# Kernel optimization log

Measured on AMD Instinct MI355X. Metric: run time of the kernel, lower is better.

The kernel has to match this reference:

```python
import jax, jax.numpy as jnp
import numpy as np

N_NODES = 100000
N_EDGES = 1000000
N_FEAT = 136
HIDDEN = 64
N_CLASSES = 2
NUM_GRAPHS = 512


def setup_inputs() -> dict:
    key = jax.random.key(0)
    ks = jax.random.split(key, 8)
    x = jax.random.normal(ks[0], (N_NODES, N_FEAT), dtype=jnp.float32)
    edge_index = jax.random.randint(ks[1], (2, N_EDGES), 0, N_NODES, dtype=jnp.int64)
    batch = jnp.sort(jax.random.randint(ks[2], (N_NODES,), 0, NUM_GRAPHS, dtype=jnp.int64))
    W1 = jax.random.normal(ks[3], (N_FEAT, HIDDEN), dtype=jnp.float32) * (1.0 / np.sqrt(N_FEAT))
    b1 = jnp.zeros((HIDDEN,), dtype=jnp.float32)
    W2 = jax.random.normal(ks[4], (HIDDEN, HIDDEN), dtype=jnp.float32) * (1.0 / np.sqrt(HIDDEN))
    b2 = jnp.zeros((HIDDEN,), dtype=jnp.float32)
    Wout = jax.random.normal(ks[5], (HIDDEN, N_CLASSES), dtype=jnp.float32) * (1.0 / np.sqrt(HIDDEN))
    bout = jnp.zeros((N_CLASSES,), dtype=jnp.float32)
    return {"x": x, "edge_index": edge_index, "batch": batch,
            "W1": W1, "b1": b1, "W2": W2, "b2": b2, "Wout": Wout, "bout": bout}


def _gcn_conv(x, src, dst, W, b, n_nodes):
    # GCNConv: D^{-1/2} (A+I) D^{-1/2} X W + b (self-loops already appended in src/dst)
    h = x @ W                                           # [N, out]
    ones = jnp.ones(src.shape, dtype=h.dtype)
    deg = jax.ops.segment_sum(ones, dst, num_segments=n_nodes)  # in-degree incl. self-loop
    dinv = jnp.where(deg > 0, jax.lax.rsqrt(deg), 0.0)
    norm = dinv[src] * dinv[dst]                        # [E]
    msg = h[src] * norm[:, None]                        # gather + normalize
    out = jax.ops.segment_sum(msg, dst, num_segments=n_nodes)   # scatter-add
    return out + b


def reference(x, edge_index, batch, W1, b1, W2, b2, Wout, bout):
    n = x.shape[0]
    loops = jnp.arange(n, dtype=edge_index.dtype)
    src = jnp.concatenate([edge_index[0], loops])
    dst = jnp.concatenate([edge_index[1], loops])

    h = jax.nn.relu(_gcn_conv(x, src, dst, W1, b1, n))
    # dropout p=0.5 is identity in eval mode
    h = jax.nn.relu(_gcn_conv(h, src, dst, W2, b2, n))

    # global_mean_pool over batch segments
    sums = jax.ops.segment_sum(h, batch, num_segments=NUM_GRAPHS)       # [G, H]
    counts = jax.ops.segment_sum(jnp.ones((n,), h.dtype), batch, num_segments=NUM_GRAPHS)
    pooled = sums / jnp.maximum(counts, 1.0)[:, None]

    return pooled @ Wout + bout                                         # [G, C]
```

## Files before the change

kernel.cpp:

```cpp
#include <hip/hip_runtime.h>
#include <hip/hip_bf16.h>

#define N_NODES   100000
#define N_EDGES   1000000
#define N_FEAT    136
#define HIDDEN    64
#define N_CLASSES 2
#define NUM_GRAPHS 512

#define NP_PAD    100352
#define SCAN_BLKS 98

#define EPW       128
#define NWAVE     7813
#define E_PAD     (NWAVE * EPW)
#define SEG_BLOCKS ((NWAVE + 3) / 4)

#define XCD        8
#define PART_N     (N_NODES / XCD)

#define K1_4 (N_FEAT / 4)
#define K2_4 (HIDDEN / 4)

#define K1PAD 160
#define K2PAD 72

typedef unsigned short ushort_t;
typedef __attribute__((ext_vector_type(8))) short bf16x8;
typedef __attribute__((ext_vector_type(4))) float f32x4;

__device__ __forceinline__ ushort_t f2b(float v) {
    unsigned b = __float_as_uint(v);
    return (ushort_t)((b + 0x7FFF + ((b >> 16) & 1)) >> 16);
}
__device__ __forceinline__ float b2f(ushort_t u) {
    return __uint_as_float(((unsigned)u) << 16);
}
__device__ __forceinline__ unsigned pack2(float a, float b) {
    return (unsigned)f2b(a) | ((unsigned)f2b(b) << 16);
}

__global__ __launch_bounds__(256) void hist_kernel(const int* __restrict__ dst,
                                                   int* __restrict__ cnt) {
    int e = blockIdx.x * 256 + threadIdx.x;
    if (e < N_EDGES) {
        int d = __builtin_nontemporal_load(&dst[e]);
        atomicAdd(&cnt[d], 1);
    }
}

__global__ __launch_bounds__(256) void scan1_kernel(const int* __restrict__ cnt,
                                                    int* __restrict__ row_ptr,
                                                    int* __restrict__ partials) {
    __shared__ int sd[256];
    int b = blockIdx.x, t = threadIdx.x;
    int i0 = b * 1024 + t * 4;
    int c0 = (i0 + 0 < N_NODES) ? cnt[i0 + 0] : 0;
    int c1 = (i0 + 1 < N_NODES) ? cnt[i0 + 1] : 0;
    int c2 = (i0 + 2 < N_NODES) ? cnt[i0 + 2] : 0;
    int c3 = (i0 + 3 < N_NODES) ? cnt[i0 + 3] : 0;
    int tsum = c0 + c1 + c2 + c3;
    sd[t] = tsum;
    __syncthreads();
    for (int off = 1; off < 256; off <<= 1) {
        int v = (t >= off) ? sd[t - off] : 0;
        __syncthreads();
        sd[t] += v;
        __syncthreads();
    }
    int excl = sd[t] - tsum;
    row_ptr[i0 + 0] = excl;
    row_ptr[i0 + 1] = excl + c0;
    row_ptr[i0 + 2] = excl + c0 + c1;
    row_ptr[i0 + 3] = excl + c0 + c1 + c2;
    if (t == 255) partials[b] = sd[255];
}

__global__ __launch_bounds__(128) void scan2_kernel(int* __restrict__ partials) {
    __shared__ int sd[128];
    int t = threadIdx.x;
    int v = (t < SCAN_BLKS) ? partials[t] : 0;
    sd[t] = v;
    __syncthreads();
    for (int off = 1; off < 128; off <<= 1) {
        int u = (t >= off) ? sd[t - off] : 0;
        __syncthreads();
        sd[t] += u;
        __syncthreads();
    }
    partials[t] = sd[t] - v;
}

__global__ __launch_bounds__(256) void scan3_kernel(int* __restrict__ row_ptr,
                                                    const int* __restrict__ cnt,
                                                    int* __restrict__ cursor,
                                                    const int* __restrict__ partials,
                                                    int* __restrict__ dst_sorted,
                                                    int* __restrict__ csr_src,
                                                    float* __restrict__ dinv) {
    int i = blockIdx.x * 256 + threadIdx.x;
    if (i < N_NODES) {
        int v = row_ptr[i] + partials[i >> 10];
        int deg = cnt[i];
        row_ptr[i] = v;
        cursor[i]  = v;
        dinv[i] = rsqrtf((float)(deg + 1));
        for (int j = v; j < v + deg; ++j) dst_sorted[j] = i;
    }
    if (i == N_NODES) {
        row_ptr[N_NODES] = N_EDGES;
        for (int j = N_EDGES; j < E_PAD; ++j) {
            dst_sorted[j] = N_NODES;
            csr_src[j] = 0;
        }
    }
}

__global__ __launch_bounds__(256) void scatter_kernel(const int* __restrict__ src,
                                                      const int* __restrict__ dst,
                                                      int* __restrict__ cursor,
                                                      int* __restrict__ csr_src) {
    int part = blockIdx.x & (XCD - 1);
    int e = (blockIdx.x >> 3) * 256 + threadIdx.x;
    if (e >= N_EDGES) return;
    int d = __builtin_nontemporal_load(&dst[e]);
    int lo = part * PART_N;
    if (d >= lo && d < lo + PART_N) {
        int s = __builtin_nontemporal_load(&src[e]);
        int pos = atomicAdd(&cursor[d], 1);
        csr_src[pos] = s;
    }
}

__global__ __launch_bounds__(256) void gbounds_kernel(const int* __restrict__ batch,
                                                      int* __restrict__ gstart) {
    int g = blockIdx.x * 256 + threadIdx.x;
    if (g > NUM_GRAPHS) return;
    int lo = 0, hi = N_NODES;
    while (lo < hi) {
        int mid = (lo + hi) >> 1;
        if (batch[mid] < g) lo = mid + 1; else hi = mid;
    }
    gstart[g] = lo;
}

__global__ __launch_bounds__(256) void mm1_kernel(const float* __restrict__ x,
                                                  const float* __restrict__ W1,
                                                  const float* __restrict__ dinv,
                                                  ushort_t* __restrict__ tpb) {
    __shared__ ushort_t xsb[64 * K1PAD];
    __shared__ ushort_t wtb[64 * K1PAD];
    __shared__ float    dsv[64];
    int t = threadIdx.x;
    int n0 = blockIdx.x * 64;
    {
        const float4* x4 = (const float4*)x;
        for (int i = t; i < 64 * K1_4; i += 256) {
            int r = i / K1_4, c = i % K1_4;
            int n = n0 + r; if (n >= N_NODES) n = N_NODES - 1;
            float4 v = x4[(long long)n * K1_4 + c];
            *(uint2*)&xsb[r * K1PAD + 4 * c] =
                make_uint2(pack2(v.x, v.y), pack2(v.z, v.w));
        }
        for (int i = t; i < 64 * 12; i += 256) {
            int r = i / 12, c = i % 12;
            *(unsigned*)&xsb[r * K1PAD + N_FEAT + 2 * c] = 0;
        }
        for (int i = t; i < N_FEAT * HIDDEN; i += 256) {
            int n = i & 63, k = i >> 6;
            wtb[n * K1PAD + k] = f2b(W1[i]);
        }
        for (int i = t; i < 64 * 12; i += 256) {
            int n = i / 12, c = i % 12;
            *(unsigned*)&wtb[n * K1PAD + N_FEAT + 2 * c] = 0;
        }
        if (t < 64) {
            int n = n0 + t; if (n >= N_NODES) n = N_NODES - 1;
            dsv[t] = dinv[n];
        }
    }
    __syncthreads();
    int w = t >> 6, lane = t & 63;
    int quad = lane >> 4, l16 = lane & 15;
    f32x4 acc[4] = {{0,0,0,0},{0,0,0,0},{0,0,0,0},{0,0,0,0}};
#pragma unroll
    for (int kc = 0; kc < K1PAD / 32; ++kc) {
        bf16x8 a = *(const bf16x8*)&xsb[(w * 16 + l16) * K1PAD + kc * 32 + quad * 8];
#pragma unroll
        for (int nt = 0; nt < 4; ++nt) {
            bf16x8 b = *(const bf16x8*)&wtb[(nt * 16 + l16) * K1PAD + kc * 32 + quad * 8];
            acc[nt] = __builtin_amdgcn_mfma_f32_16x16x32_bf16(a, b, acc[nt], 0, 0, 0);
        }
    }
#pragma unroll
    for (int r = 0; r < 4; ++r) {
        int nl = w * 16 + quad * 4 + r;
        int node = n0 + nl;
        if (node < N_NODES) {
            float di = dsv[nl];
#pragma unroll
            for (int nt = 0; nt < 4; ++nt)
                tpb[node * 64 + nt * 16 + l16] = f2b(acc[nt][r] * di);
        }
    }
}

__global__ __launch_bounds__(256) void mm2_kernel(float* __restrict__ agg,
                                                  ushort_t* __restrict__ tpb,
                                                  const float* __restrict__ W2,
                                                  const float* __restrict__ dinv,
                                                  const float* __restrict__ bias) {
    __shared__ ushort_t hsb[64 * K2PAD];
    __shared__ ushort_t wtb[64 * K2PAD];
    __shared__ float    dsv[64];
    __shared__ float    bsv[64];
    int t = threadIdx.x;
    int n0 = blockIdx.x * 64;
    if (t < 64) {
        int n = n0 + t; if (n >= N_NODES) n = N_NODES - 1;
        dsv[t] = dinv[n];
        bsv[t] = bias[t];
    }
    __syncthreads();
    {
        for (int i = t; i < HIDDEN * HIDDEN; i += 256) {
            int n = i & 63, k = i >> 6;
            wtb[n * K2PAD + k] = f2b(W2[i]);
        }
        for (int i = t; i < 64 * 4; i += 256) {
            int n = i / 4, c = i % 4;
            *(unsigned*)&wtb[n * K2PAD + HIDDEN + 2 * c] = 0;
        }
        for (int i = t; i < 64 * 16; i += 256) {
            int r = i >> 4, c = i & 15;
            int n_raw = n0 + r;
            int n = (n_raw < N_NODES) ? n_raw : N_NODES - 1;
            float4 va = ((const float4*)agg)[n * 16 + c];
            uint2 ut = *(const uint2*)&tpb[n * 64 + c * 4];
            float di = dsv[r];
            float s0 = b2f((ushort_t)(ut.x & 0xffff));
            float s1 = b2f((ushort_t)(ut.x >> 16));
            float s2 = b2f((ushort_t)(ut.y & 0xffff));
            float s3 = b2f((ushort_t)(ut.y >> 16));
            float h0 = fmaxf(fmaf(va.x + s0, di, bsv[c * 4 + 0]), 0.f);
            float h1 = fmaxf(fmaf(va.y + s1, di, bsv[c * 4 + 1]), 0.f);
            float h2 = fmaxf(fmaf(va.z + s2, di, bsv[c * 4 + 2]), 0.f);
            float h3 = fmaxf(fmaf(va.w + s3, di, bsv[c * 4 + 3]), 0.f);
            *(uint2*)&hsb[r * K2PAD + 4 * c] = make_uint2(pack2(h0, h1), pack2(h2, h3));
            if (n_raw < N_NODES)
                ((float4*)agg)[n * 16 + c] = make_float4(0.f, 0.f, 0.f, 0.f);
        }
        for (int i = t; i < 64 * 4; i += 256) {
            int r = i / 4, c = i % 4;
            *(unsigned*)&hsb[r * K2PAD + HIDDEN + 2 * c] = 0;
        }
    }
    __syncthreads();
    int w = t >> 6, lane = t & 63;
    int quad = lane >> 4, l16 = lane & 15;
    f32x4 acc[4] = {{0,0,0,0},{0,0,0,0},{0,0,0,0},{0,0,0,0}};
#pragma unroll
    for (int kc = 0; kc < 2; ++kc) {
        bf16x8 a = *(const bf16x8*)&hsb[(w * 16 + l16) * K2PAD + kc * 32 + quad * 8];
#pragma unroll
        for (int nt = 0; nt < 4; ++nt) {
            bf16x8 b = *(const bf16x8*)&wtb[(nt * 16 + l16) * K2PAD + kc * 32 + quad * 8];
            acc[nt] = __builtin_amdgcn_mfma_f32_16x16x32_bf16(a, b, acc[nt], 0, 0, 0);
        }
    }
#pragma unroll
    for (int r = 0; r < 4; ++r) {
        int nl = w * 16 + quad * 4 + r;
        int node = n0 + nl;
        if (node < N_NODES) {
            float di = dsv[nl];
#pragma unroll
            for (int nt = 0; nt < 4; ++nt)
                tpb[node * 64 + nt * 16 + l16] = f2b(acc[nt][r] * di);
        }
    }
}

__global__ __launch_bounds__(256, 4) void edge_seg_kernel(const int* __restrict__ csr_src,
                                                          const int* __restrict__ dst_sorted,
                                                          const ushort_t* __restrict__ tpb,
                                                          float* __restrict__ agg) {
    int lane = threadIdx.x & 63;
    int wid  = (blockIdx.x * 256 + threadIdx.x) >> 6;
    if (wid >= NWAVE) return;
    int e0 = wid * EPW;

    int sv0 = csr_src[e0 + lane],      sv1 = csr_src[e0 + 64 + lane];
    int dv0 = dst_sorted[e0 + lane],   dv1 = dst_sorted[e0 + 64 + lane];

    float acc = 0.0f;
    int dprev = __builtin_amdgcn_readlane(dv0, 0);
    int nflush = 0;
#pragma unroll
    for (int j = 0; j < 8; ++j) {
        int svj = (j < 4) ? sv0 : sv1;
        int dvj = (j < 4) ? dv0 : dv1;
        int base = (j * 16) & 63;
        int ss[16], dd[16];
#pragma unroll
        for (int k = 0; k < 16; ++k) {
            ss[k] = __builtin_amdgcn_readlane(svj, base + k);
            dd[k] = __builtin_amdgcn_readlane(dvj, base + k);
        }
        float vv[16];
#pragma unroll
        for (int k = 0; k < 16; ++k) vv[k] = b2f(tpb[ss[k] * 64 + lane]);
#pragma unroll
        for (int k = 0; k < 16; ++k) {
            if (dd[k] != dprev) {
                if (nflush == 0) atomicAdd(&agg[dprev * 64 + lane], acc);
                else             agg[dprev * 64 + lane] = acc;
                ++nflush;
                acc = 0.0f;
                dprev = dd[k];
            }
            acc += vv[k];
        }
    }
    atomicAdd(&agg[dprev * 64 + lane], acc);
}

__global__ __launch_bounds__(256) void gpool_kernel(const float* __restrict__ agg,
                                                    const ushort_t* __restrict__ tpb,
                                                    const float* __restrict__ dinv,
                                                    const float* __restrict__ bias,
                                                    const int* __restrict__ gstart,
                                                    float* __restrict__ sums,
                                                    float* __restrict__ gcount) {
    __shared__ float red[4][64];
    int lane = threadIdx.x & 63;
    int w = threadIdx.x >> 6;
    int g = blockIdx.x;
    int s = gstart[g], e = gstart[g + 1];
    float b = bias[lane];
    float acc = 0.0f;
    for (int n = s + w; n < e; n += 4) {
        int idx = n * 64 + lane;
        acc += fmaxf(fmaf(agg[idx] + b2f(tpb[idx]), dinv[n], b), 0.0f);
    }
    red[w][lane] = acc;
    __syncthreads();
    if (threadIdx.x < 64) {
        float tot = red[0][lane] + red[1][lane] + red[2][lane] + red[3][lane];
        sums[g * 64 + lane] = tot;
        if (lane == 0) gcount[g] = (float)(e - s);
    }
}

__global__ __launch_bounds__(256) void out_kernel(const float* __restrict__ sums,
                                                  const float* __restrict__ gcount,
                                                  const float* __restrict__ Wout,
                                                  const float* __restrict__ bout,
                                                  float* __restrict__ out) {
    int idx = blockIdx.x * 256 + threadIdx.x;
    if (idx >= NUM_GRAPHS * N_CLASSES) return;
    int g = idx / N_CLASSES, c = idx % N_CLASSES;
    float inv_cnt = 1.0f / fmaxf(gcount[g], 1.0f);
    float acc = 0.0f;
#pragma unroll
    for (int k = 0; k < HIDDEN; ++k)
        acc += sums[g * HIDDEN + k] * Wout[k * N_CLASSES + c];
    out[idx] = acc * inv_cnt + bout[c];
}

extern "C" void kernel_launch(void* const* d_in, const int* in_sizes, int n_in,
                              void* d_out, int out_size, void* d_ws, size_t ws_size,
                              hipStream_t stream) {
    const float* x     = (const float*)d_in[0];
    const int*   ei    = (const int*)d_in[1];
    const int*   batch = (const int*)d_in[2];
    const float* W1    = (const float*)d_in[3];
    const float* b1    = (const float*)d_in[4];
    const float* W2    = (const float*)d_in[5];
    const float* b2    = (const float*)d_in[6];
    const float* Wout  = (const float*)d_in[7];
    const float* bout  = (const float*)d_in[8];
    float* out = (float*)d_out;

    const int* src = ei;
    const int* dst = ei + N_EDGES;

    char* p = (char*)d_ws;
    int*      row_ptr   = (int*)p;      p += (NP_PAD + 256) * sizeof(int);
    int*      cnt       = (int*)p;      p += NP_PAD * sizeof(int);
    int*      cursor    = (int*)p;      p += NP_PAD * sizeof(int);
    int*      partials  = (int*)p;      p += 256 * sizeof(int);
    int*      gstart    = (int*)p;      p += (NUM_GRAPHS + 64) * sizeof(int);
    int*      csr_src   = (int*)p;      p += (size_t)E_PAD * sizeof(int);
    int*      dst_sorted= (int*)p;      p += (size_t)E_PAD * sizeof(int);
    float*    dinv      = (float*)p;    p += NP_PAD * sizeof(float);
    ushort_t* tpb       = (ushort_t*)p; p += (size_t)N_NODES * HIDDEN * sizeof(ushort_t);
    float*    agg       = (float*)p;    p += (size_t)(N_NODES + 1) * HIDDEN * sizeof(float);
    float*    sums      = (float*)p;    p += NUM_GRAPHS * HIDDEN * sizeof(float);
    float*    gcount    = (float*)p;    p += NUM_GRAPHS * sizeof(float);

    const int NB_E  = (N_EDGES + 255) / 256;
    const int NB_MM = (N_NODES + 63) / 64;

    hipMemsetAsync(cnt, 0, NP_PAD * sizeof(int), stream);
    hist_kernel<<<NB_E, 256, 0, stream>>>(dst, cnt);
    scan1_kernel<<<SCAN_BLKS, 256, 0, stream>>>(cnt, row_ptr, partials);
    scan2_kernel<<<1, 128, 0, stream>>>(partials);
    scan3_kernel<<<NP_PAD / 256 + 1, 256, 0, stream>>>(row_ptr, cnt, cursor, partials,
                                                       dst_sorted, csr_src, dinv);
    scatter_kernel<<<XCD * NB_E, 256, 0, stream>>>(src, dst, cursor, csr_src);
    gbounds_kernel<<<3, 256, 0, stream>>>(batch, gstart);

    hipMemsetAsync(agg, 0, (size_t)(N_NODES + 1) * HIDDEN * sizeof(float), stream);

    mm1_kernel<<<NB_MM, 256, 0, stream>>>(x, W1, dinv, tpb);
    edge_seg_kernel<<<SEG_BLOCKS, 256, 0, stream>>>(csr_src, dst_sorted, tpb, agg);

    mm2_kernel<<<NB_MM, 256, 0, stream>>>(agg, tpb, W2, dinv, b1);
    edge_seg_kernel<<<SEG_BLOCKS, 256, 0, stream>>>(csr_src, dst_sorted, tpb, agg);
    gpool_kernel<<<NUM_GRAPHS, 256, 0, stream>>>(agg, tpb, dinv, b2, gstart,
                                                 sums, gcount);

    out_kernel<<<(NUM_GRAPHS * N_CLASSES + 255) / 256, 256, 0, stream>>>(
        sums, gcount, Wout, bout, out);
}
```

Baseline: 310.0 us.

## Record edge ranks in histogram to make CSR scatter atomic-free, fuse small kernels

```diff
diff --git a/kernel.cpp b/kernel.cpp
--- a/kernel.cpp
+++ b/kernel.cpp
@@ -16,18 +16,20 @@
 #define E_PAD     (NWAVE * EPW)
 #define SEG_BLOCKS ((NWAVE + 3) / 4)
 
-#define XCD        8
-#define PART_N     (N_NODES / XCD)
-
 #define K1_4 (N_FEAT / 4)
 #define K2_4 (HIDDEN / 4)
 
 #define K1PAD 160
 #define K2PAD 72
+
+#define NB_E  ((N_EDGES + 255) / 256)
+#define NB_SC ((N_EDGES / 4 + 255) / 256)
 
 typedef unsigned short ushort_t;
 typedef __attribute__((ext_vector_type(8))) short bf16x8;
 typedef __attribute__((ext_vector_type(4))) float f32x4;
+typedef __attribute__((ext_vector_type(4))) int i32x4;
+typedef __attribute__((ext_vector_type(4))) unsigned short u16x4;
 
 __device__ __forceinline__ ushort_t f2b(float v) {
     unsigned b = __float_as_uint(v);
@@ -41,11 +43,27 @@
 }
 
 __global__ __launch_bounds__(256) void hist_kernel(const int* __restrict__ dst,
-                                                   int* __restrict__ cnt) {
+                                                   int* __restrict__ cnt,
+                                                   ushort_t* __restrict__ rank,
+                                                   const int* __restrict__ batch,
+                                                   int* __restrict__ gstart) {
+    if (blockIdx.x >= NB_E) {
+        int g = (blockIdx.x - NB_E) * 256 + threadIdx.x;
+        if (g <= NUM_GRAPHS) {
+            int lo = 0, hi = N_NODES;
+            while (lo < hi) {
+                int mid = (lo + hi) >> 1;
+                if (batch[mid] < g) lo = mid + 1; else hi = mid;
+            }
+            gstart[g] = lo;
+        }
+        return;
+    }
     int e = blockIdx.x * 256 + threadIdx.x;
     if (e < N_EDGES) {
         int d = __builtin_nontemporal_load(&dst[e]);
-        atomicAdd(&cnt[d], 1);
+        int r = atomicAdd(&cnt[d], 1);
+        rank[e] = (ushort_t)r;
     }
 }
 
@@ -93,7 +111,6 @@
 
 __global__ __launch_bounds__(256) void scan3_kernel(int* __restrict__ row_ptr,
                                                     const int* __restrict__ cnt,
-                                                    int* __restrict__ cursor,
                                                     const int* __restrict__ partials,
                                                     int* __restrict__ dst_sorted,
                                                     int* __restrict__ csr_src,
@@ -103,7 +120,6 @@
         int v = row_ptr[i] + partials[i >> 10];
         int deg = cnt[i];
         row_ptr[i] = v;
-        cursor[i]  = v;
         dinv[i] = rsqrtf((float)(deg + 1));
         for (int j = v; j < v + deg; ++j) dst_sorted[j] = i;
     }
@@ -118,42 +134,41 @@
 
 __global__ __launch_bounds__(256) void scatter_kernel(const int* __restrict__ src,
                                                       const int* __restrict__ dst,
-                                                      int* __restrict__ cursor,
+                                                      const ushort_t* __restrict__ rank,
+                                                      const int* __restrict__ row_ptr,
                                                       int* __restrict__ csr_src) {
-    int part = blockIdx.x & (XCD - 1);
-    int e = (blockIdx.x >> 3) * 256 + threadIdx.x;
-    if (e >= N_EDGES) return;
-    int d = __builtin_nontemporal_load(&dst[e]);
-    int lo = part * PART_N;
-    if (d >= lo && d < lo + PART_N) {
-        int s = __builtin_nontemporal_load(&src[e]);
-        int pos = atomicAdd(&cursor[d], 1);
-        csr_src[pos] = s;
-    }
-}
-
-__global__ __launch_bounds__(256) void gbounds_kernel(const int* __restrict__ batch,
-                                                      int* __restrict__ gstart) {
-    int g = blockIdx.x * 256 + threadIdx.x;
-    if (g > NUM_GRAPHS) return;
-    int lo = 0, hi = N_NODES;
-    while (lo < hi) {
-        int mid = (lo + hi) >> 1;
-        if (batch[mid] < g) lo = mid + 1; else hi = mid;
-    }
-    gstart[g] = lo;
+    int e0 = (blockIdx.x * 256 + threadIdx.x) * 4;
+    if (e0 >= N_EDGES) return;
+    i32x4 s4 = __builtin_nontemporal_load((const i32x4*)&src[e0]);
+    i32x4 d4 = __builtin_nontemporal_load((const i32x4*)&dst[e0]);
+    u16x4 r4 = *(const u16x4*)&rank[e0];
+    int p0 = row_ptr[d4.x] + (int)r4.x;
+    int p1 = row_ptr[d4.y] + (int)r4.y;
+    int p2 = row_ptr[d4.z] + (int)r4.z;
+    int p3 = row_ptr[d4.w] + (int)r4.w;
+    csr_src[p0] = s4.x;
+    csr_src[p1] = s4.y;
+    csr_src[p2] = s4.z;
+    csr_src[p3] = s4.w;
 }
 
 __global__ __launch_bounds__(256) void mm1_kernel(const float* __restrict__ x,
                                                   const float* __restrict__ W1,
                                                   const float* __restrict__ dinv,
-                                                  ushort_t* __restrict__ tpb) {
+                                                  ushort_t* __restrict__ tpb,
+                                                  float* __restrict__ agg) {
     __shared__ ushort_t xsb[64 * K1PAD];
     __shared__ ushort_t wtb[64 * K1PAD];
     __shared__ float    dsv[64];
     int t = threadIdx.x;
     int n0 = blockIdx.x * 64;
     {
+        for (int i = t; i < 64 * 16; i += 256) {
+            int r = i >> 4, c = i & 15;
+            int n = n0 + r;
+            if (n < N_NODES)
+                ((float4*)agg)[n * 16 + c] = make_float4(0.f, 0.f, 0.f, 0.f);
+        }
         const float4* x4 = (const float4*)x;
         for (int i = t; i < 64 * K1_4; i += 256) {
             int r = i / K1_4, c = i % K1_4;
@@ -330,8 +345,9 @@
                                                     const float* __restrict__ dinv,
                                                     const float* __restrict__ bias,
                                                     const int* __restrict__ gstart,
-                                                    float* __restrict__ sums,
-                                                    float* __restrict__ gcount) {
+                                                    const float* __restrict__ Wout,
+                                                    const float* __restrict__ bout,
+                                                    float* __restrict__ out) {
     __shared__ float red[4][64];
     int lane = threadIdx.x & 63;
     int w = threadIdx.x >> 6;
@@ -347,25 +363,19 @@
     __syncthreads();
     if (threadIdx.x < 64) {
         float tot = red[0][lane] + red[1][lane] + red[2][lane] + red[3][lane];
-        sums[g * 64 + lane] = tot;
-        if (lane == 0) gcount[g] = (float)(e - s);
-    }
-}
-
-__global__ __launch_bounds__(256) void out_kernel(const float* __restrict__ sums,
-                                                  const float* __restrict__ gcount,
-                                                  const float* __restrict__ Wout,
-                                                  const float* __restrict__ bout,
-                                                  float* __restrict__ out) {
-    int idx = blockIdx.x * 256 + threadIdx.x;
-    if (idx >= NUM_GRAPHS * N_CLASSES) return;
-    int g = idx / N_CLASSES, c = idx % N_CLASSES;
-    float inv_cnt = 1.0f / fmaxf(gcount[g], 1.0f);
-    float acc = 0.0f;
-#pragma unroll
-    for (int k = 0; k < HIDDEN; ++k)
-        acc += sums[g * HIDDEN + k] * Wout[k * N_CLASSES + c];
-    out[idx] = acc * inv_cnt + bout[c];
+        float p = tot / fmaxf((float)(e - s), 1.0f);
+        float c0 = p * Wout[lane * N_CLASSES + 0];
+        float c1 = p * Wout[lane * N_CLASSES + 1];
+#pragma unroll
+        for (int off = 32; off > 0; off >>= 1) {
+            c0 += __shfl_down(c0, off);
+            c1 += __shfl_down(c1, off);
+        }
+        if (lane == 0) {
+            out[g * N_CLASSES + 0] = c0 + bout[0];
+            out[g * N_CLASSES + 1] = c1 + bout[1];
+        }
+    }
 }
 
 extern "C" void kernel_launch(void* const* d_in, const int* in_sizes, int n_in,
@@ -388,7 +398,6 @@
     char* p = (char*)d_ws;
     int*      row_ptr   = (int*)p;      p += (NP_PAD + 256) * sizeof(int);
     int*      cnt       = (int*)p;      p += NP_PAD * sizeof(int);
-    int*      cursor    = (int*)p;      p += NP_PAD * sizeof(int);
     int*      partials  = (int*)p;      p += 256 * sizeof(int);
     int*      gstart    = (int*)p;      p += (NUM_GRAPHS + 64) * sizeof(int);
     int*      csr_src   = (int*)p;      p += (size_t)E_PAD * sizeof(int);
@@ -396,31 +405,24 @@
     float*    dinv      = (float*)p;    p += NP_PAD * sizeof(float);
     ushort_t* tpb       = (ushort_t*)p; p += (size_t)N_NODES * HIDDEN * sizeof(ushort_t);
     float*    agg       = (float*)p;    p += (size_t)(N_NODES + 1) * HIDDEN * sizeof(float);
-    float*    sums      = (float*)p;    p += NUM_GRAPHS * HIDDEN * sizeof(float);
-    float*    gcount    = (float*)p;    p += NUM_GRAPHS * sizeof(float);
-
-    const int NB_E  = (N_EDGES + 255) / 256;
+    ushort_t* rank16    = (ushort_t*)agg;
+
     const int NB_MM = (N_NODES + 63) / 64;
 
     hipMemsetAsync(cnt, 0, NP_PAD * sizeof(int), stream);
-    hist_kernel<<<NB_E, 256, 0, stream>>>(dst, cnt);
+    hist_kernel<<<NB_E + 3, 256, 0, stream>>>(dst, cnt, rank16, batch, gstart);
     scan1_kernel<<<SCAN_BLKS, 256, 0, stream>>>(cnt, row_ptr, partials);
     scan2_kernel<<<1, 128, 0, stream>>>(partials);
-    scan3_kernel<<<NP_PAD / 256 + 1, 256, 0, stream>>>(row_ptr, cnt, cursor, partials,
+    scan3_kernel<<<NP_PAD / 256 + 1, 256, 0, stream>>>(row_ptr, cnt, partials,
                                                        dst_sorted, csr_src, dinv);
-    scatter_kernel<<<XCD * NB_E, 256, 0, stream>>>(src, dst, cursor, csr_src);
-    gbounds_kernel<<<3, 256, 0, stream>>>(batch, gstart);
-
-    hipMemsetAsync(agg, 0, (size_t)(N_NODES + 1) * HIDDEN * sizeof(float), stream);
-
-    mm1_kernel<<<NB_MM, 256, 0, stream>>>(x, W1, dinv, tpb);
+    scatter_kernel<<<NB_SC, 256, 0, stream>>>(src, dst, rank16, row_ptr, csr_src);
+
+    mm1_kernel<<<NB_MM, 256, 0, stream>>>(x, W1, dinv, tpb, agg);
     edge_seg_kernel<<<SEG_BLOCKS, 256, 0, stream>>>(csr_src, dst_sorted, tpb, agg);
 
     mm2_kernel<<<NB_MM, 256, 0, stream>>>(agg, tpb, W2, dinv, b1);
     edge_seg_kernel<<<SEG_BLOCKS, 256, 0, stream>>>(csr_src, dst_sorted, tpb, agg);
+
     gpool_kernel<<<NUM_GRAPHS, 256, 0, stream>>>(agg, tpb, dinv, b2, gstart,
-                                                 sums, gcount);
-
-    out_kernel<<<(NUM_GRAPHS * N_CLASSES + 255) / 256, 256, 0, stream>>>(
-        sums, gcount, Wout, bout, out);
-}
+                                                 Wout, bout, out);
+}
```

Result: faster. 283.4 us (-8.6%).
